# Optimization experiments

Measured on AMD Instinct MI355X. Metric: run time of the kernel, lower is better.

The kernel has to match this reference:

```python
import jax, jax.numpy as jnp
import numpy as np

H = 15

def setup_inputs() -> dict:
    key = jax.random.key(0)
    ks = jax.random.split(key, 9)
    N = 2097152
    return {
        "x": jax.random.normal(ks[0], (N, 2), dtype=jnp.float32),
        "W1": jax.random.normal(ks[1], (2, H), dtype=jnp.float32) * (1.0 / np.sqrt(2)),
        "b1": jax.random.normal(ks[2], (H,), dtype=jnp.float32) * 0.1,
        "W2": jax.random.normal(ks[3], (H, H), dtype=jnp.float32) * (1.0 / np.sqrt(H)),
        "b2": jax.random.normal(ks[4], (H,), dtype=jnp.float32) * 0.1,
        "W3": jax.random.normal(ks[5], (H, H), dtype=jnp.float32) * (1.0 / np.sqrt(H)),
        "b3": jax.random.normal(ks[6], (H,), dtype=jnp.float32) * 0.1,
        "W4": jax.random.normal(ks[7], (H, 1), dtype=jnp.float32) * (1.0 / np.sqrt(H)),
        "b4": jax.random.normal(ks[8], (1,), dtype=jnp.float32) * 0.1,
    }

def reference(x, W1, b1, W2, b2, W3, b3, W4, b4):
    # Linear(2,H) -> SiLU -> Linear(H,H) -> SiLU -> Linear(H,H) -> SiLU -> Linear(H,1) -> Sigmoid
    h = jax.nn.silu(x @ W1 + b1)      # [N, H]
    h = jax.nn.silu(h @ W2 + b2)      # [N, H]
    h = jax.nn.silu(h @ W3 + b3)      # [N, H]
    return jax.nn.sigmoid(h @ W4 + b4)  # [N, 1]
```

## Files before the change

kernel.cpp:

```cpp
#include <hip/hip_runtime.h>


using half4   = __attribute__((ext_vector_type(4))) _Float16;
using half2v  = __attribute__((ext_vector_type(2))) _Float16;
using fp16x2  = __attribute__((ext_vector_type(2))) __fp16;
using floatx4 = __attribute__((ext_vector_type(4))) float;
using v2f     = __attribute__((ext_vector_type(2))) float;

__device__ __forceinline__ v2f sigmoid2(v2f x) {
    v2f e;
    e[0] = __expf(-x[0]);
    e[1] = __expf(-x[1]);
    v2f den = e + 1.0f;
    v2f r;
    r[0] = __builtin_amdgcn_rcpf(den[0]);
    r[1] = __builtin_amdgcn_rcpf(den[1]);
    return r;
}

__device__ __forceinline__ half2v silu2h(v2f x) {
    v2f s = x * sigmoid2(x);
    fp16x2 p = __builtin_amdgcn_cvt_pkrtz(s[0], s[1]);
    return __builtin_bit_cast(half2v, p);
}

__global__ __launch_bounds__(256) void mlp_mfma(
    const float* __restrict__ x,
    const float* __restrict__ W1, const float* __restrict__ b1,
    const float* __restrict__ W2, const float* __restrict__ b2,
    const float* __restrict__ W3, const float* __restrict__ b3,
    const float* __restrict__ W4, const float* __restrict__ b4,
    float* __restrict__ out, int N)
{
    const int lane = threadIdx.x & 63;
    const int col  = lane & 15;
    const int quad = lane >> 4;

    half4 A2, A3, A4;
    v2f w10p[2], w11p[2], vb1p[2];
    v2f vb2p[2], vb3p[2];
    #pragma unroll
    for (int i = 0; i < 4; ++i) {
        const int k    = quad * 4 + i;
        const int m    = col;
        const bool kin = (k < 15);
        A2[i] = (_Float16)((kin && m < 15) ? W2[k * 15 + m] : 0.0f);
        A3[i] = (_Float16)((kin && m < 15) ? W3[k * 15 + m] : 0.0f);
        A4[i] = (_Float16)((kin && m == 0) ? W4[k]          : 0.0f);
        w10p[i >> 1][i & 1] = kin ? W1[0 * 15 + k] : 0.0f;
        w11p[i >> 1][i & 1] = kin ? W1[1 * 15 + k] : 0.0f;
        vb1p[i >> 1][i & 1] = kin ? b1[k] : 0.0f;
        const int mq = quad * 4 + i;
        vb2p[i >> 1][i & 1] = (mq < 15) ? b2[mq] : 0.0f;
        vb3p[i >> 1][i & 1] = (mq < 15) ? b3[mq] : 0.0f;
    }
    const float b4s = b4[0];
    const floatx4 zero = {0.f, 0.f, 0.f, 0.f};

    const int wave   = (blockIdx.x * blockDim.x + threadIdx.x) >> 6;
    const int nwaves = (gridDim.x * blockDim.x) >> 6;
    const int npairs = N >> 5;

    for (int p = wave; p < npairs; p += nwaves) {
        const int base0 = p * 32;
        const int base1 = base0 + 16;
        const float2 xv0 = *reinterpret_cast<const float2*>(x + 2 * (base0 + col));
        const float2 xv1 = *reinterpret_cast<const float2*>(x + 2 * (base1 + col));

        half4 B0, B1v;
        #pragma unroll
        for (int j = 0; j < 2; ++j) {
            v2f a0 = w10p[j] * xv0.x + (w11p[j] * xv0.y + vb1p[j]);
            v2f a1 = w10p[j] * xv1.x + (w11p[j] * xv1.y + vb1p[j]);
            half2v p0 = silu2h(a0);
            half2v p1 = silu2h(a1);
            B0[2*j]  = p0[0]; B0[2*j+1]  = p0[1];
            B1v[2*j] = p1[0]; B1v[2*j+1] = p1[1];
        }

        floatx4 d0 = __builtin_amdgcn_mfma_f32_16x16x16f16(A2, B0,  zero, 0, 0, 0);
        floatx4 d1 = __builtin_amdgcn_mfma_f32_16x16x16f16(A2, B1v, zero, 0, 0, 0);
        #pragma unroll
        for (int j = 0; j < 2; ++j) {
            v2f t0 = (v2f){d0[2*j], d0[2*j+1]} + vb2p[j];
            v2f t1 = (v2f){d1[2*j], d1[2*j+1]} + vb2p[j];
            half2v p0 = silu2h(t0);
            half2v p1 = silu2h(t1);
            B0[2*j]  = p0[0]; B0[2*j+1]  = p0[1];
            B1v[2*j] = p1[0]; B1v[2*j+1] = p1[1];
        }

        d0 = __builtin_amdgcn_mfma_f32_16x16x16f16(A3, B0,  zero, 0, 0, 0);
        d1 = __builtin_amdgcn_mfma_f32_16x16x16f16(A3, B1v, zero, 0, 0, 0);
        #pragma unroll
        for (int j = 0; j < 2; ++j) {
            v2f t0 = (v2f){d0[2*j], d0[2*j+1]} + vb3p[j];
            v2f t1 = (v2f){d1[2*j], d1[2*j+1]} + vb3p[j];
            half2v p0 = silu2h(t0);
            half2v p1 = silu2h(t1);
            B0[2*j]  = p0[0]; B0[2*j+1]  = p0[1];
            B1v[2*j] = p1[0]; B1v[2*j+1] = p1[1];
        }

        d0 = __builtin_amdgcn_mfma_f32_16x16x16f16(A4, B0,  zero, 0, 0, 0);
        d1 = __builtin_amdgcn_mfma_f32_16x16x16f16(A4, B1v, zero, 0, 0, 0);

        v2f o = (v2f){d0[0], d1[0]} + b4s;
        v2f s = sigmoid2(o);
        if (lane < 16) {
            out[base0 + lane] = s[0];
            out[base1 + lane] = s[1];
        }
    }
}

extern "C" void kernel_launch(void* const* d_in, const int* in_sizes, int n_in,
                              void* d_out, int out_size, void* d_ws, size_t ws_size,
                              hipStream_t stream) {
    const float* x  = (const float*)d_in[0];
    const float* W1 = (const float*)d_in[1];
    const float* b1 = (const float*)d_in[2];
    const float* W2 = (const float*)d_in[3];
    const float* b2 = (const float*)d_in[4];
    const float* W3 = (const float*)d_in[5];
    const float* b3 = (const float*)d_in[6];
    const float* W4 = (const float*)d_in[7];
    const float* b4 = (const float*)d_in[8];
    float* out = (float*)d_out;

    const int N = in_sizes[0] / 2;
    const int blocks = 2048;
    mlp_mfma<<<blocks, 256, 0, stream>>>(x, W1, b1, W2, b2, W3, b3, W4, b4, out, N);
}
```

Before: 111.8 us.

## Process four tiles per iteration with x prefetch and paired reciprocal sigmoid

Each wave now handles 64 rows per loop iteration as four independent MFMA chains instead of two, and loads the next iteration's x values before computing the current one, so load latency is hidden behind compute. The sigmoid now computes two reciprocals with a single rcp of the product of the denominators, cutting transcendental ops. Launch bounds add a minimum of four blocks per CU, which limits register use. The shared reciprocal can overflow or underflow when both denominators are large, and more live registers may cause spills.

```diff
diff --git a/kernel.cpp b/kernel.cpp
--- a/kernel.cpp
+++ b/kernel.cpp
@@ -8,14 +8,11 @@
 using v2f     = __attribute__((ext_vector_type(2))) float;
 
 __device__ __forceinline__ v2f sigmoid2(v2f x) {
-    v2f e;
-    e[0] = __expf(-x[0]);
-    e[1] = __expf(-x[1]);
-    v2f den = e + 1.0f;
-    v2f r;
-    r[0] = __builtin_amdgcn_rcpf(den[0]);
-    r[1] = __builtin_amdgcn_rcpf(den[1]);
-    return r;
+    v2f den;
+    den[0] = 1.0f + __expf(-x[0]);
+    den[1] = 1.0f + __expf(-x[1]);
+    const float r = __builtin_amdgcn_rcpf(den[0] * den[1]);
+    return (v2f){den[1] * r, den[0] * r};
 }
 
 __device__ __forceinline__ half2v silu2h(v2f x) {
@@ -24,7 +21,7 @@
     return __builtin_bit_cast(half2v, p);
 }
 
-__global__ __launch_bounds__(256) void mlp_mfma(
+__global__ __launch_bounds__(256, 4) void mlp_mfma(
     const float* __restrict__ x,
     const float* __restrict__ W1, const float* __restrict__ b1,
     const float* __restrict__ W2, const float* __restrict__ b2,
@@ -59,58 +56,79 @@
 
     const int wave   = (blockIdx.x * blockDim.x + threadIdx.x) >> 6;
     const int nwaves = (gridDim.x * blockDim.x) >> 6;
-    const int npairs = N >> 5;
+    const int nquads = N >> 6;
 
-    for (int p = wave; p < npairs; p += nwaves) {
-        const int base0 = p * 32;
-        const int base1 = base0 + 16;
-        const float2 xv0 = *reinterpret_cast<const float2*>(x + 2 * (base0 + col));
-        const float2 xv1 = *reinterpret_cast<const float2*>(x + 2 * (base1 + col));
+    if (wave >= nquads) return;
 
-        half4 B0, B1v;
+    float2 xc[4];
+    #pragma unroll
+    for (int t = 0; t < 4; ++t)
+        xc[t] = *reinterpret_cast<const float2*>(x + 2 * (wave * 64 + t * 16 + col));
+
+    for (int q = wave; q < nquads; ) {
+        const int qn   = q + nwaves;
+        const int qp   = (qn < nquads) ? qn : q;
+        float2 xn[4];
         #pragma unroll
-        for (int j = 0; j < 2; ++j) {
-            v2f a0 = w10p[j] * xv0.x + (w11p[j] * xv0.y + vb1p[j]);
-            v2f a1 = w10p[j] * xv1.x + (w11p[j] * xv1.y + vb1p[j]);
-            half2v p0 = silu2h(a0);
-            half2v p1 = silu2h(a1);
-            B0[2*j]  = p0[0]; B0[2*j+1]  = p0[1];
-            B1v[2*j] = p1[0]; B1v[2*j+1] = p1[1];
+        for (int t = 0; t < 4; ++t)
+            xn[t] = *reinterpret_cast<const float2*>(x + 2 * (qp * 64 + t * 16 + col));
+
+        half4 B[4];
+        #pragma unroll
+        for (int t = 0; t < 4; ++t) {
+            #pragma unroll
+            for (int j = 0; j < 2; ++j) {
+                v2f a = w10p[j] * xc[t].x + (w11p[j] * xc[t].y + vb1p[j]);
+                half2v p = silu2h(a);
+                B[t][2*j] = p[0]; B[t][2*j+1] = p[1];
+            }
         }
 
-        floatx4 d0 = __builtin_amdgcn_mfma_f32_16x16x16f16(A2, B0,  zero, 0, 0, 0);
-        floatx4 d1 = __builtin_amdgcn_mfma_f32_16x16x16f16(A2, B1v, zero, 0, 0, 0);
+        floatx4 d[4];
         #pragma unroll
-        for (int j = 0; j < 2; ++j) {
-            v2f t0 = (v2f){d0[2*j], d0[2*j+1]} + vb2p[j];
-            v2f t1 = (v2f){d1[2*j], d1[2*j+1]} + vb2p[j];
-            half2v p0 = silu2h(t0);
-            half2v p1 = silu2h(t1);
-            B0[2*j]  = p0[0]; B0[2*j+1]  = p0[1];
-            B1v[2*j] = p1[0]; B1v[2*j+1] = p1[1];
+        for (int t = 0; t < 4; ++t)
+            d[t] = __builtin_amdgcn_mfma_f32_16x16x16f16(A2, B[t], zero, 0, 0, 0);
+        #pragma unroll
+        for (int t = 0; t < 4; ++t) {
+            #pragma unroll
+            for (int j = 0; j < 2; ++j) {
+                v2f tt = (v2f){d[t][2*j], d[t][2*j+1]} + vb2p[j];
+                half2v p = silu2h(tt);
+                B[t][2*j] = p[0]; B[t][2*j+1] = p[1];
+            }
         }
 
-        d0 = __builtin_amdgcn_mfma_f32_16x16x16f16(A3, B0,  zero, 0, 0, 0);
-        d1 = __builtin_amdgcn_mfma_f32_16x16x16f16(A3, B1v, zero, 0, 0, 0);
         #pragma unroll
-        for (int j = 0; j < 2; ++j) {
-            v2f t0 = (v2f){d0[2*j], d0[2*j+1]} + vb3p[j];
-            v2f t1 = (v2f){d1[2*j], d1[2*j+1]} + vb3p[j];
-            half2v p0 = silu2h(t0);
-            half2v p1 = silu2h(t1);
-            B0[2*j]  = p0[0]; B0[2*j+1]  = p0[1];
-            B1v[2*j] = p1[0]; B1v[2*j+1] = p1[1];
+        for (int t = 0; t < 4; ++t)
+            d[t] = __builtin_amdgcn_mfma_f32_16x16x16f16(A3, B[t], zero, 0, 0, 0);
+        #pragma unroll
+        for (int t = 0; t < 4; ++t) {
+            #pragma unroll
+            for (int j = 0; j < 2; ++j) {
+                v2f tt = (v2f){d[t][2*j], d[t][2*j+1]} + vb3p[j];
+                half2v p = silu2h(tt);
+                B[t][2*j] = p[0]; B[t][2*j+1] = p[1];
+            }
         }
 
-        d0 = __builtin_amdgcn_mfma_f32_16x16x16f16(A4, B0,  zero, 0, 0, 0);
-        d1 = __builtin_amdgcn_mfma_f32_16x16x16f16(A4, B1v, zero, 0, 0, 0);
+        #pragma unroll
+        for (int t = 0; t < 4; ++t)
+            d[t] = __builtin_amdgcn_mfma_f32_16x16x16f16(A4, B[t], zero, 0, 0, 0);
 
-        v2f o = (v2f){d0[0], d1[0]} + b4s;
-        v2f s = sigmoid2(o);
+        v2f o01 = (v2f){d[0][0], d[1][0]} + b4s;
+        v2f o23 = (v2f){d[2][0], d[3][0]} + b4s;
+        v2f s01 = sigmoid2(o01);
+        v2f s23 = sigmoid2(o23);
         if (lane < 16) {
-            out[base0 + lane] = s[0];
-            out[base1 + lane] = s[1];
+            out[q * 64 +  0 + lane] = s01[0];
+            out[q * 64 + 16 + lane] = s01[1];
+            out[q * 64 + 32 + lane] = s23[0];
+            out[q * 64 + 48 + lane] = s23[1];
         }
+
+        q = qn;
+        #pragma unroll
+        for (int t = 0; t < 4; ++t) xc[t] = xn[t];
     }
 }
 
```

After: 108.9 us. 2.6% less time.

## Share one reciprocal across sigmoid pairs, vectorize x loads/stores, add occupancy hint

Applied to the files above, without the earlier changes.

The paired sigmoid now computes one reciprocal of the product of both denominators and recovers each value by multiplying by the other denominator, halving the rcp transcendental count. Each lane now takes two adjacent rows through a single float4 load, and the two outputs are written with one float2 store, which replaces the two interleaved 16-row halves. Launch bounds also request 8 waves per EU. The risks are overflow of the denominator product for very negative inputs (inf leading to 0/NaN results) and register pressure from the occupancy hint.

```diff
diff --git a/kernel.cpp b/kernel.cpp
--- a/kernel.cpp
+++ b/kernel.cpp
@@ -8,14 +8,11 @@
 using v2f     = __attribute__((ext_vector_type(2))) float;
 
 __device__ __forceinline__ v2f sigmoid2(v2f x) {
-    v2f e;
-    e[0] = __expf(-x[0]);
-    e[1] = __expf(-x[1]);
-    v2f den = e + 1.0f;
-    v2f r;
-    r[0] = __builtin_amdgcn_rcpf(den[0]);
-    r[1] = __builtin_amdgcn_rcpf(den[1]);
-    return r;
+    v2f den;
+    den[0] = 1.0f + __expf(-x[0]);
+    den[1] = 1.0f + __expf(-x[1]);
+    const float r = __builtin_amdgcn_rcpf(den[0] * den[1]);
+    return (v2f){den[1] * r, den[0] * r};
 }
 
 __device__ __forceinline__ half2v silu2h(v2f x) {
@@ -24,7 +21,7 @@
     return __builtin_bit_cast(half2v, p);
 }
 
-__global__ __launch_bounds__(256) void mlp_mfma(
+__global__ __launch_bounds__(256, 8) void mlp_mfma(
     const float* __restrict__ x,
     const float* __restrict__ W1, const float* __restrict__ b1,
     const float* __restrict__ W2, const float* __restrict__ b2,
@@ -57,21 +54,19 @@
     const float b4s = b4[0];
     const floatx4 zero = {0.f, 0.f, 0.f, 0.f};
 
-    const int wave   = (blockIdx.x * blockDim.x + threadIdx.x) >> 6;
-    const int nwaves = (gridDim.x * blockDim.x) >> 6;
-    const int npairs = N >> 5;
+    const int wave    = (blockIdx.x * blockDim.x + threadIdx.x) >> 6;
+    const int nwaves  = (gridDim.x * blockDim.x) >> 6;
+    const int nchunks = N >> 5;
 
-    for (int p = wave; p < npairs; p += nwaves) {
-        const int base0 = p * 32;
-        const int base1 = base0 + 16;
-        const float2 xv0 = *reinterpret_cast<const float2*>(x + 2 * (base0 + col));
-        const float2 xv1 = *reinterpret_cast<const float2*>(x + 2 * (base1 + col));
+    for (int q = wave; q < nchunks; q += nwaves) {
+        const int base = q * 32;
+        const float4 xv = *reinterpret_cast<const float4*>(x + 2 * (base + 2 * col));
 
         half4 B0, B1v;
         #pragma unroll
         for (int j = 0; j < 2; ++j) {
-            v2f a0 = w10p[j] * xv0.x + (w11p[j] * xv0.y + vb1p[j]);
-            v2f a1 = w10p[j] * xv1.x + (w11p[j] * xv1.y + vb1p[j]);
+            v2f a0 = w10p[j] * xv.x + (w11p[j] * xv.y + vb1p[j]);
+            v2f a1 = w10p[j] * xv.z + (w11p[j] * xv.w + vb1p[j]);
             half2v p0 = silu2h(a0);
             half2v p1 = silu2h(a1);
             B0[2*j]  = p0[0]; B0[2*j+1]  = p0[1];
@@ -108,8 +103,7 @@
         v2f o = (v2f){d0[0], d1[0]} + b4s;
         v2f s = sigmoid2(o);
         if (lane < 16) {
-            out[base0 + lane] = s[0];
-            out[base1 + lane] = s[1];
+            *reinterpret_cast<float2*>(out + base + 2 * lane) = (float2){s[0], s[1]};
         }
     }
 }
```

Result: faster. 109.2 us (-2.3%).
